# Kernel tuning notes

Hardware: AMD Instinct MI355X
Metric: run time of the kernel (lower is better)

## Reference

```python
import jax, jax.numpy as jnp
import numpy as np

WINDOW = 16      # window_size[0]
LANDM_H = 8      # closest_square_factors(64) = (8, 8)
LANDM_W = 8
MAX_VAL = 5.0
PINV_ITERS = 6


def activ(x):
    # ExpLinearAfterThreshold: exp(clamp(x, max=5)) + relu(x - 5)
    return jnp.exp(jnp.minimum(x, MAX_VAL)) + jax.nn.relu(x - MAX_VAL)


def pool_landmarks(x):
    # x: [B, H, N, d] with N = WINDOW*WINDOW.
    B, H, N, d = x.shape
    kh, kw = WINDOW // LANDM_H, WINDOW // LANDM_W
    x = x.reshape(B, H, LANDM_H, kh, LANDM_W, kw, d)
    return x.mean(axis=(3, 5)).reshape(B, H, LANDM_H * LANDM_W, d)  # [B, H, L, d]


def moore_penrose_pinv(x, iters=PINV_ITERS):
    # x: [B, H, L, L]
    abs_x = jnp.abs(x)
    col = abs_x.sum(axis=-1)
    row = abs_x.sum(axis=-2)
    z = jnp.swapaxes(x, -1, -2) / (jnp.max(col) * jnp.max(row) + 1e-15)
    I = jnp.eye(x.shape[-1], dtype=x.dtype)
    for _ in range(iters):
        xz = x @ z
        z = 0.25 * z @ (13.0 * I - xz @ (15.0 * I - xz @ (7.0 * I - xz)))
    return z


def setup_inputs() -> dict:
    key = jax.random.key(0)
    kq, kk, kv = jax.random.split(key, 3)
    shape = (256, 16, 256, 64)  # [B_, num_heads, window^2, head_dim]
    q = jax.random.normal(kq, shape, dtype=jnp.float32)
    k = jax.random.normal(kk, shape, dtype=jnp.float32)
    v = jax.random.normal(kv, shape, dtype=jnp.float32)
    return {"q": q, "k": k, "v": v}


def reference(q, k, v):
    # q, k, v: [B, H, N, d]
    q_m = pool_landmarks(q)  # [B, H, L, d]
    k_m = pool_landmarks(k)  # [B, H, L, d]

    temp = activ(jnp.einsum('bhld,bhmd->bhlm', q_m, k_m))   # [B, H, L, L]
    pinv = moore_penrose_pinv(temp, PINV_ITERS)              # [B, H, L, L]

    # kernel(q_m, k) @ [v | 1]  -> [B, H, L, d+1]
    v1 = jnp.concatenate([v, jnp.ones_like(v[..., :1])], axis=-1)
    kv = jnp.einsum('bhln,bhne->bhle', activ(jnp.einsum('bhld,bhnd->bhln', q_m, k)), v1)

    # kernel(q, k_m) @ pinv @ kv  -> [B, H, N, d+1]
    qk = activ(jnp.einsum('bhnd,bhld->bhnl', q, k_m))        # [B, H, N, L]
    prod = jnp.einsum('bhnl,bhle->bhne', qk @ pinv, kv)

    return prod[..., :-1] / (prod[..., -1:] + 1e-12)
```

## Files before the change

kernel.cpp:

```cpp
#include <hip/hip_runtime.h>
#include <math.h>


#define G_TOT 4096
#define TPB_R 256
#define TPB_M 1024
typedef _Float16 f16;
typedef __attribute__((ext_vector_type(2))) _Float16 f16x2;
typedef __attribute__((ext_vector_type(4))) _Float16 f16x4;
typedef __attribute__((ext_vector_type(8))) _Float16 f16x8;
typedef __attribute__((ext_vector_type(4))) float f32x4;
typedef __attribute__((ext_vector_type(16))) float f32x16;

#define NPLANES 16
#define SMEM_BYTES (NPLANES * 4096 * 2 + 320 * 4)

#define LSCALE 2048.0f
#define LINV   (1.0f / 2048.0f)
#define ZS     1024.0f
#define ZINV   (1.0f / 1024.0f)

struct HL { f16 h, l; };
__device__ __forceinline__ HL split2(float v) {
    HL r;
    r.h = (f16)v;
    r.l = (f16)((v - (float)r.h) * LSCALE);
    return r;
}
__device__ __forceinline__ float join2(f16 h, f16 l) {
    return (float)h + (float)l * LINV;
}
__device__ __forceinline__ int swi(int r, int c) {
    return (r << 6) + (c ^ ((r & 7) << 3));
}
__device__ __forceinline__ float activ_f(float x) {
    return __expf(fminf(x, 5.0f)) + fmaxf(x - 5.0f, 0.0f);
}
__device__ __forceinline__ float activ_r(float x) {
    return expf(fminf(x, 5.0f)) + fmaxf(x - 5.0f, 0.0f);
}
__device__ __forceinline__ void split_w(f16* Ph, f16* Pl, int r, int c, float v) {
    HL s = split2(v);
    const int o = swi(r, c);
    Ph[o] = s.h;
    Pl[o] = s.l;
}
__device__ __forceinline__ f16x2 mk2(f16 a, f16 b) { f16x2 r; r[0]=a; r[1]=b; return r; }
__device__ __forceinline__ f16x4 mk4(f16 a, f16 b, f16 c, f16 d) { f16x4 r; r[0]=a;r[1]=b;r[2]=c;r[3]=d; return r; }
__device__ __forceinline__ f32x4 z4() { f32x4 z = {0.f,0.f,0.f,0.f}; return z; }
__device__ __forceinline__ f32x16 z16() {
    f32x16 z;
#pragma unroll
    for (int i = 0; i < 16; ++i) z[i] = 0.f;
    return z;
}

struct Frag { f16x8 h[2], l[2]; };

__device__ __forceinline__ Frag ld_frag(const f16* __restrict__ Ph,
                                        const f16* __restrict__ Pl,
                                        int row, int kg) {
    Frag f;
    const int base = row << 6, x = (row & 7) << 3;
#pragma unroll
    for (int s = 0; s < 2; ++s) {
        const int o = base + ((((s << 5) + (kg << 3))) ^ x);
        f.h[s] = *(const f16x8*)(Ph + o);
        f.l[s] = *(const f16x8*)(Pl + o);
    }
    return f;
}

__device__ __forceinline__ f32x4 mm16_rr(const Frag& A, const Frag& B, f32x4 acc) {
    f32x4 ax1 = z4(), ax2 = z4();
#pragma unroll
    for (int s = 0; s < 2; ++s) {
        acc = __builtin_amdgcn_mfma_f32_16x16x32_f16(A.h[s], B.h[s], acc, 0, 0, 0);
        ax1 = __builtin_amdgcn_mfma_f32_16x16x32_f16(A.h[s], B.l[s], ax1, 0, 0, 0);
        ax2 = __builtin_amdgcn_mfma_f32_16x16x32_f16(A.l[s], B.h[s], ax2, 0, 0, 0);
    }
    acc += (ax1 + ax2) * LINV;
    return acc;
}

__device__ __forceinline__ void wfrag_rm(f16* Ph, f16* Pl, int Rb, int C, const float* v) {
#pragma unroll
    for (int m = 0; m < 4; ++m) split_w(Ph, Pl, Rb + m, C, v[m]);
}
__device__ __forceinline__ void wfrag_t(f16* Ph, f16* Pl, int Rb, int C, const float* v) {
    const int o = swi(C, Rb);
    HL s0 = split2(v[0]), s1 = split2(v[1]), s2 = split2(v[2]), s3 = split2(v[3]);
    *(f16x4*)(Ph + o) = mk4(s0.h, s1.h, s2.h, s3.h);
    *(f16x4*)(Pl + o) = mk4(s0.l, s1.l, s2.l, s3.l);
}

__device__ __forceinline__ void wr_rm(float4 vv, f16* Ph, f16* Pl, int t) {
    const int r = t >> 4, c4 = (t & 15) << 2;
    const int o = swi(r, c4);
    HL s0 = split2(vv.x), s1 = split2(vv.y), s2 = split2(vv.z), s3 = split2(vv.w);
    *(f16x4*)(Ph + o) = mk4(s0.h, s1.h, s2.h, s3.h);
    *(f16x4*)(Pl + o) = mk4(s0.l, s1.l, s2.l, s3.l);
}
__device__ __forceinline__ void ld_vt(const float* __restrict__ src, int t,
                                      float2& va, float2& vb) {
    const int n0 = (t >> 5) << 1, e0 = (t & 31) << 1;
    va = *(const float2*)(src + (size_t)n0 * 64 + e0);
    vb = *(const float2*)(src + (size_t)(n0 + 1) * 64 + e0);
}
__device__ __forceinline__ void wr_vt(float2 va, float2 vb, f16* Ph, f16* Pl, int t) {
    const int n0 = (t >> 5) << 1, e0 = (t & 31) << 1;
    HL ax = split2(va.x), ay = split2(va.y), bx = split2(vb.x), by = split2(vb.y);
    const int o0 = swi(e0, n0), o1 = swi(e0 + 1, n0);
    *(f16x2*)(Ph + o0) = mk2(ax.h, bx.h);
    *(f16x2*)(Pl + o0) = mk2(ax.l, bx.l);
    *(f16x2*)(Ph + o1) = mk2(ay.h, by.h);
    *(f16x2*)(Pl + o1) = mk2(ay.l, by.l);
}

__device__ __forceinline__ void pool_global1024(const float* __restrict__ src,
                                                f16* Ph, f16* Pl, int t) {
    const int L = t >> 4, d0 = (t & 15) << 2;
    const int nb = ((L >> 3) << 5) + ((L & 7) << 1);
    const float* p = src + (size_t)nb * 64 + d0;
    float4 a = *(const float4*)p;
    float4 b = *(const float4*)(p + 64);
    float4 c = *(const float4*)(p + 1024);
    float4 d = *(const float4*)(p + 1088);
    HL s0 = split2(0.25f * (a.x + b.x + c.x + d.x));
    HL s1 = split2(0.25f * (a.y + b.y + c.y + d.y));
    HL s2 = split2(0.25f * (a.z + b.z + c.z + d.z));
    HL s3 = split2(0.25f * (a.w + b.w + c.w + d.w));
    const int o = swi(L, d0);
    *(f16x4*)(Ph + o) = mk4(s0.h, s1.h, s2.h, s3.h);
    *(f16x4*)(Pl + o) = mk4(s0.l, s1.l, s2.l, s3.l);
}

__device__ __forceinline__ void pool_lds512(const f16* Kh, const f16* Kl,
                                            f16* Ph, f16* Pl, int t, int tt) {
    const int ll = t >> 5, d0 = (t & 31) << 1;
    const int rb = ((ll >> 3) << 5) + ((ll & 7) << 1);
    float s0 = 0.f, s1 = 0.f;
#pragma unroll
    for (int rr = 0; rr < 4; ++rr) {
        const int r = rb + (rr & 1) + ((rr >> 1) << 4);
        const int o = swi(r, d0);
        f16x2 h = *(const f16x2*)(Kh + o);
        f16x2 l = *(const f16x2*)(Kl + o);
        s0 += join2(h[0], l[0]);
        s1 += join2(h[1], l[1]);
    }
    const int L = (tt << 4) + ll;
    HL p0 = split2(0.25f * s0), p1 = split2(0.25f * s1);
    const int o = swi(L, d0);
    *(f16x2*)(Ph + o) = mk2(p0.h, p1.h);
    *(f16x2*)(Pl + o) = mk2(p0.l, p1.l);
}

__device__ __forceinline__ f32x16 mm64q(const f16* __restrict__ Ah, const f16* __restrict__ Al,
                                        const f16* __restrict__ Bh, const f16* __restrict__ Bl,
                                        int lane, int wr, int wc, f32x16 acc) {
    const int cl = lane & 31, hh = lane >> 5;
    const int ar = (wr << 5) + cl, br = (wc << 5) + cl;
    const int abase = ar << 6, axor = (ar & 7) << 3;
    const int bbase = br << 6, bxor = (br & 7) << 3;
    f32x16 ax1 = z16();
    f32x16 ax2 = z16();
#pragma unroll
    for (int ks = 0; ks < 4; ++ks) {
        const int k0 = (ks << 4) + (hh << 3);
        const int ao = abase + (k0 ^ axor);
        const int bo = bbase + (k0 ^ bxor);
        f16x8 a_h = *(const f16x8*)(Ah + ao);
        f16x8 a_l = *(const f16x8*)(Al + ao);
        f16x8 b_h = *(const f16x8*)(Bh + bo);
        f16x8 b_l = *(const f16x8*)(Bl + bo);
        acc = __builtin_amdgcn_mfma_f32_32x32x16_f16(a_h, b_h, acc, 0, 0, 0);
        ax1 = __builtin_amdgcn_mfma_f32_32x32x16_f16(a_h, b_l, ax1, 0, 0, 0);
        ax2 = __builtin_amdgcn_mfma_f32_32x32x16_f16(a_l, b_h, ax2, 0, 0, 0);
    }
    acc += (ax1 + ax2) * LINV;
    return acc;
}
__device__ __forceinline__ void pool_global_r(const float* __restrict__ src,
                                              f16* Ph, f16* Pl, int t) {
    const int ll = t >> 4, d0 = (t & 15) << 2;
    const int rb = ((ll >> 3) << 5) + ((ll & 7) << 1);
#pragma unroll
    for (int tt = 0; tt < 4; ++tt) {
        const float* p = src + (size_t)((tt << 6) + rb) * 64 + d0;
        float4 a = *(const float4*)p;
        float4 b = *(const float4*)(p + 64);
        float4 c = *(const float4*)(p + 1024);
        float4 d = *(const float4*)(p + 1088);
        const int L = (tt << 4) + ll;
        split_w(Ph, Pl, L, d0 + 0, 0.25f * (a.x + b.x + c.x + d.x));
        split_w(Ph, Pl, L, d0 + 1, 0.25f * (a.y + b.y + c.y + d.y));
        split_w(Ph, Pl, L, d0 + 2, 0.25f * (a.z + b.z + c.z + d.z));
        split_w(Ph, Pl, L, d0 + 3, 0.25f * (a.w + b.w + c.w + d.w));
    }
}

#define WAVE_SUM32(v)            \
    v += __shfl_xor(v, 1);       \
    v += __shfl_xor(v, 2);       \
    v += __shfl_xor(v, 4);       \
    v += __shfl_xor(v, 8);       \
    v += __shfl_xor(v, 16);

__global__ void k_init(float* ws) {
    if (threadIdx.x < 2) ws[threadIdx.x] = 0.0f;
}

__global__ __launch_bounds__(TPB_R) void k_reduce(const float* __restrict__ q,
                                                  const float* __restrict__ k,
                                                  float* __restrict__ ws) {
    __shared__ f16 pls[4 * 4096];
    __shared__ float rowS[64], colS[64];
    const int t = threadIdx.x, g = blockIdx.x;
    const int lane = t & 63, wv = t >> 6, wr = wv >> 1, wc = wv & 1;
    const int cl = lane & 31, hh = lane >> 5;
    if (t < 64) rowS[t] = 0.f;
    else if (t < 128) colS[t - 64] = 0.f;
    pool_global_r(q + (size_t)g * 16384, pls, pls + 4096, t);
    pool_global_r(k + (size_t)g * 16384, pls + 8192, pls + 12288, t);
    __syncthreads();
    f32x16 a = mm64q(pls, pls + 4096, pls + 8192, pls + 12288, lane, wr, wc, z16());
    float colp = 0.f;
#pragma unroll
    for (int m = 0; m < 16; ++m) {
        float x = activ_r(a[m]);
        const int R = (wr << 5) + (m & 3) + ((m >> 2) << 3) + (hh << 2);
        float vs = x;
        WAVE_SUM32(vs)
        if (cl == 0) atomicAdd(&rowS[R], vs);
        colp += x;
    }
    colp += __shfl_xor(colp, 32);
    if (hh == 0) atomicAdd(&colS[(wc << 5) + cl], colp);
    __syncthreads();
    if (t < 64) {
        float vmx = rowS[t];
        for (int off = 1; off < 64; off <<= 1) vmx = fmaxf(vmx, __shfl_xor(vmx, off));
        if (t == 0) atomicMax((int*)ws, __float_as_int(vmx));
    } else if (t < 128) {
        float vmx = colS[t - 64];
        for (int off = 1; off < 64; off <<= 1) vmx = fmaxf(vmx, __shfl_xor(vmx, off));
        if (t == 64) atomicMax(((int*)ws) + 1, __float_as_int(vmx));
    }
}

__global__ __launch_bounds__(TPB_M, 4) void k_main(const float* __restrict__ q,
                                                   const float* __restrict__ k,
                                                   const float* __restrict__ v,
                                                   const float* __restrict__ ws,
                                                   float* __restrict__ out) {
    extern __shared__ f16 smu[];
    float* kv1 = (float*)(smu + NPLANES * 4096);
    float* den = kv1 + 64;
    const int t = threadIdx.x, g = blockIdx.x;
    const int lane = t & 63, w = t >> 6;
    const int ti = w & 3, tj = w >> 2;
    const int fr = lane & 15, kg = lane >> 4;
    const int arow = (ti << 4) + fr;
    const int brow = (tj << 4) + fr;
    const int C = brow;
    const int Rb = (ti << 4) + (kg << 2);
    const float* Gq = q + (size_t)g * 16384;
    const float* Gk = k + (size_t)g * 16384;
    const float* Gv = v + (size_t)g * 16384;
    float* og = out + (size_t)g * 16384;

    f16* Xh  = smu +  0 * 4096; f16* Xl  = smu +  1 * 4096;
    f16* SAh = smu +  2 * 4096; f16* SAl = smu +  3 * 4096;
    f16* SBh = smu +  4 * 4096; f16* SBl = smu +  5 * 4096;
    f16* KMh = smu +  6 * 4096; f16* KMl = smu +  7 * 4096;
    f16* SCh = smu +  8 * 4096; f16* SCl = smu +  9 * 4096;
    f16* KVh = smu + 10 * 4096; f16* KVl = smu + 11 * 4096;
    f16* Z0rh= smu + 12 * 4096; f16* Z0rl= smu + 13 * 4096;
    f16* Z0th= smu + 14 * 4096; f16* Z0tl= smu + 15 * 4096;

    if (t < 320) kv1[t] = 0.f;
    pool_global1024(Gq, Z0rh, Z0rl, t);
    {
        float4 kreg = *(const float4*)(Gk + (size_t)t * 4);
        float2 va, vb; ld_vt(Gv, t, va, vb);
        wr_rm(kreg, SAh, SAl, t);
        wr_vt(va, vb, SBh, SBl, t);
    }
    __syncthreads();

    Frag fQM = ld_frag(Z0rh, Z0rl, arow, kg);

    f32x4 kva = z4();
    for (int tt = 0; tt < 4; ++tt) {
        f16* vch = (tt & 1) ? Xh : SBh;  f16* vcl = (tt & 1) ? Xl : SBl;
        f16* vnh = (tt & 1) ? SBh : Xh;  f16* vnl = (tt & 1) ? SBl : Xl;
        float4 kregN; float2 vaN, vbN;
        if (tt < 3) {
            kregN = *(const float4*)(Gk + (size_t)(tt + 1) * 4096 + (size_t)t * 4);
            ld_vt(Gv + (size_t)(tt + 1) * 4096, t, vaN, vbN);
        }
        if (t < 512) pool_lds512(SAh, SAl, KMh, KMl, t, tt);
        {
            Frag bK = ld_frag(SAh, SAl, brow, kg);
            f32x4 s = mm16_rr(fQM, bK, z4());
            float sv[4];
#pragma unroll
            for (int m = 0; m < 4; ++m) {
                sv[m] = activ_f(s[m]);
                float vs = sv[m];
                vs += __shfl_xor(vs, 1); vs += __shfl_xor(vs, 2);
                vs += __shfl_xor(vs, 4); vs += __shfl_xor(vs, 8);
                if (fr == 0) atomicAdd(&kv1[Rb + m], vs);
            }
            wfrag_rm(SCh, SCl, Rb, C, sv);
        }
        if (tt < 3) wr_vt(vaN, vbN, vnh, vnl, t);
        __syncthreads();
        {
            Frag aS = ld_frag(SCh, SCl, arow, kg);
            Frag bV = ld_frag(vch, vcl, brow, kg);
            kva = mm16_rr(aS, bV, kva);
        }
        if (tt < 3) wr_rm(kregN, SAh, SAl, t);
        __syncthreads();
    }

    {
        float kvv[4] = {kva[0], kva[1], kva[2], kva[3]};
        wfrag_t(KVh, KVl, Rb, C, kvv);
        Frag fKMb = ld_frag(KMh, KMl, brow, kg);
        f32x4 x0 = mm16_rr(fQM, fKMb, z4());
        const float scale = ZS / (ws[0] * ws[1] + 1e-15f);
        float xv[4], zv[4];
#pragma unroll
        for (int m = 0; m < 4; ++m) { xv[m] = activ_f(x0[m]); zv[m] = xv[m] * scale; }
        wfrag_rm(Xh, Xl, Rb, C, xv);
        wfrag_t (Z0rh, Z0rl, Rb, C, zv);
        wfrag_rm(Z0th, Z0tl, Rb, C, zv);
    }
    __syncthreads();

    Frag fX = ld_frag(Xh, Xl, arow, kg);
    f16 *zrh = Z0rh, *zrl = Z0rl, *zth = Z0th, *ztl = Z0tl;
    f16 *nrh = SAh,  *nrl = SAl,  *nth = SCh,  *ntl = SCl;
#pragma unroll
    for (int it = 0; it < 6; ++it) {
        Frag bz = ld_frag(zth, ztl, brow, kg);
        f32x4 a1 = mm16_rr(fX, bz, z4());
        float t1k[4];
#pragma unroll
        for (int m = 0; m < 4; ++m) t1k[m] = a1[m] * ZINV;
        wfrag_rm(nrh, nrl, Rb, C, t1k);
        wfrag_t (nth, ntl, Rb, C, t1k);
        __syncthreads();
        Frag aT1 = ld_frag(nrh, nrl, arow, kg);
        Frag bT1 = ld_frag(nth, ntl, brow, kg);
        f32x4 a2 = mm16_rr(aT1, bT1, z4());
        float t2k[4];
#pragma unroll
        for (int m = 0; m < 4; ++m) t2k[m] = a2[m];
        wfrag_rm(Xh, Xl, Rb, C, t2k);
        __syncthreads();
        Frag aT2 = ld_frag(Xh, Xl, arow, kg);
        f32x4 a3 = mm16_rr(aT2, bT1, z4());
        float ov[4];
#pragma unroll
        for (int m = 0; m < 4; ++m) {
            const int R = Rb + m;
            ov[m] = ((R == C) ? 13.f : 0.f) - 15.f * t1k[m] + 7.f * t2k[m] - a3[m];
        }
        wfrag_t(SBh, SBl, Rb, C, ov);
        __syncthreads();
        Frag aZ = ld_frag(zrh, zrl, arow, kg);
        Frag bO = ld_frag(SBh, SBl, brow, kg);
        f32x4 a4 = mm16_rr(aZ, bO, z4());
        float zk[4];
#pragma unroll
        for (int m = 0; m < 4; ++m) zk[m] = 0.25f * a4[m];
        wfrag_rm(nrh, nrl, Rb, C, zk);
        wfrag_t (nth, ntl, Rb, C, zk);
        __syncthreads();
        f16* tp;
        tp = zrh; zrh = nrh; nrh = tp;  tp = zrl; zrl = nrl; nrl = tp;
        tp = zth; zth = nth; nth = tp;  tp = ztl; ztl = ntl; ntl = tp;
    }

    Frag fKM = ld_frag(KMh, KMl, brow, kg);
    Frag fZt = ld_frag(Z0th, Z0tl, brow, kg);
    Frag fKV = ld_frag(KVh, KVl, brow, kg);
    const float kvC = kv1[C];
    {
        float4 qreg = *(const float4*)(Gq + (size_t)t * 4);
        wr_rm(qreg, SAh, SAl, t);
    }
    __syncthreads();
    for (int tt = 0; tt < 4; ++tt) {
        float4 qregN;
        if (tt < 3) qregN = *(const float4*)(Gq + (size_t)(tt + 1) * 4096 + (size_t)t * 4);
        {
            Frag aQ = ld_frag(SAh, SAl, arow, kg);
            f32x4 q0 = mm16_rr(aQ, fKM, z4());
            float qv[4];
#pragma unroll
            for (int m = 0; m < 4; ++m) qv[m] = activ_f(q0[m]);
            wfrag_rm(SCh, SCl, Rb, C, qv);
        }
        __syncthreads();
        float* dn = den + (tt << 6);
        {
            Frag aK = ld_frag(SCh, SCl, arow, kg);
            f32x4 w0 = mm16_rr(aK, fZt, z4());
            float wv[4];
#pragma unroll
            for (int m = 0; m < 4; ++m) {
                wv[m] = w0[m] * ZINV;
                float d_ = wv[m] * kvC;
                d_ += __shfl_xor(d_, 1); d_ += __shfl_xor(d_, 2);
                d_ += __shfl_xor(d_, 4); d_ += __shfl_xor(d_, 8);
                if (fr == 0) atomicAdd(&dn[Rb + m], d_);
            }
            wfrag_rm(SBh, SBl, Rb, C, wv);
        }
        __syncthreads();
        {
            Frag aW = ld_frag(SBh, SBl, arow, kg);
            f32x4 p0 = mm16_rr(aW, fKV, z4());
#pragma unroll
            for (int m = 0; m < 4; ++m) {
                const int R = Rb + m;
                const float inv = 1.0f / (dn[R] + 1e-12f);
                og[(size_t)((tt << 6) + R) * 64 + C] = p0[m] * inv;
            }
        }
        if (tt < 3) wr_rm(qregN, SAh, SAl, t);
        __syncthreads();
    }
}

extern "C" void kernel_launch(void* const* d_in, const int* in_sizes, int n_in,
                              void* d_out, int out_size, void* d_ws, size_t ws_size,
                              hipStream_t stream) {
    const float* q = (const float*)d_in[0];
    const float* k = (const float*)d_in[1];
    const float* v = (const float*)d_in[2];
    float* out = (float*)d_out;
    float* ws  = (float*)d_ws;
    (void)in_sizes; (void)n_in; (void)out_size; (void)ws_size;

    hipFuncSetAttribute((const void*)k_main,
                        hipFuncAttributeMaxDynamicSharedMemorySize, SMEM_BYTES);

    k_init<<<1, 64, 0, stream>>>(ws);
    k_reduce<<<G_TOT, TPB_R, 0, stream>>>(q, k, ws);
    k_main<<<G_TOT, TPB_M, SMEM_BYTES, stream>>>(q, k, v, ws, out);
}
```

Measured before the change: 768.5 us.

## Process two 64-row chunks per stage to halve barrier count

The KV accumulation and output phases now handle two 64-row token chunks at once instead of looping over four chunks one at a time. Pairs of fragments are computed per barrier using spare LDS planes (SC, KV, Zt, X) as extra staging buffers. This cuts the number of __syncthreads and exposes more independent MFMA work per stage. In exchange it raises register pressure and loads more global data up front.

```diff
diff --git a/kernel.cpp b/kernel.cpp
--- a/kernel.cpp
+++ b/kernel.cpp
@@ -276,55 +276,96 @@
     f16* KMh = smu +  6 * 4096; f16* KMl = smu +  7 * 4096;
     f16* SCh = smu +  8 * 4096; f16* SCl = smu +  9 * 4096;
     f16* KVh = smu + 10 * 4096; f16* KVl = smu + 11 * 4096;
-    f16* Z0rh= smu + 12 * 4096; f16* Z0rl= smu + 13 * 4096;
-    f16* Z0th= smu + 14 * 4096; f16* Z0tl= smu + 15 * 4096;
+    f16* Zrh = smu + 12 * 4096; f16* Zrl = smu + 13 * 4096;
+    f16* Zth = smu + 14 * 4096; f16* Ztl = smu + 15 * 4096;
 
     if (t < 320) kv1[t] = 0.f;
-    pool_global1024(Gq, Z0rh, Z0rl, t);
-    {
-        float4 kreg = *(const float4*)(Gk + (size_t)t * 4);
-        float2 va, vb; ld_vt(Gv, t, va, vb);
-        wr_rm(kreg, SAh, SAl, t);
-        wr_vt(va, vb, SBh, SBl, t);
-    }
-    __syncthreads();
-
-    Frag fQM = ld_frag(Z0rh, Z0rl, arow, kg);
+    pool_global1024(Gq, Zrh, Zrl, t);
+    {
+        float4 k0 = *(const float4*)(Gk + (size_t)t * 4);
+        float4 k1 = *(const float4*)(Gk + 4096 + (size_t)t * 4);
+        float2 va0, vb0, va1, vb1;
+        ld_vt(Gv, t, va0, vb0);
+        ld_vt(Gv + 4096, t, va1, vb1);
+        wr_rm(k0, SAh, SAl, t);
+        wr_rm(k1, SCh, SCl, t);
+        wr_vt(va0, vb0, SBh, SBl, t);
+        wr_vt(va1, vb1, Xh, Xl, t);
+    }
+    __syncthreads();
+
+    Frag fQM = ld_frag(Zrh, Zrl, arow, kg);
 
     f32x4 kva = z4();
-    for (int tt = 0; tt < 4; ++tt) {
-        f16* vch = (tt & 1) ? Xh : SBh;  f16* vcl = (tt & 1) ? Xl : SBl;
-        f16* vnh = (tt & 1) ? SBh : Xh;  f16* vnl = (tt & 1) ? SBl : Xl;
-        float4 kregN; float2 vaN, vbN;
-        if (tt < 3) {
-            kregN = *(const float4*)(Gk + (size_t)(tt + 1) * 4096 + (size_t)t * 4);
-            ld_vt(Gv + (size_t)(tt + 1) * 4096, t, vaN, vbN);
-        }
-        if (t < 512) pool_lds512(SAh, SAl, KMh, KMl, t, tt);
-        {
-            Frag bK = ld_frag(SAh, SAl, brow, kg);
-            f32x4 s = mm16_rr(fQM, bK, z4());
-            float sv[4];
-#pragma unroll
-            for (int m = 0; m < 4; ++m) {
-                sv[m] = activ_f(s[m]);
-                float vs = sv[m];
-                vs += __shfl_xor(vs, 1); vs += __shfl_xor(vs, 2);
-                vs += __shfl_xor(vs, 4); vs += __shfl_xor(vs, 8);
-                if (fr == 0) atomicAdd(&kv1[Rb + m], vs);
-            }
-            wfrag_rm(SCh, SCl, Rb, C, sv);
-        }
-        if (tt < 3) wr_vt(vaN, vbN, vnh, vnl, t);
-        __syncthreads();
-        {
-            Frag aS = ld_frag(SCh, SCl, arow, kg);
-            Frag bV = ld_frag(vch, vcl, brow, kg);
-            kva = mm16_rr(aS, bV, kva);
-        }
-        if (tt < 3) wr_rm(kregN, SAh, SAl, t);
-        __syncthreads();
-    }
+    float4 kr2 = *(const float4*)(Gk + 2 * 4096 + (size_t)t * 4);
+    float4 kr3 = *(const float4*)(Gk + 3 * 4096 + (size_t)t * 4);
+    if (t < 512) pool_lds512(SAh, SAl, KMh, KMl, t, 0);
+    else         pool_lds512(SCh, SCl, KMh, KMl, t - 512, 1);
+    {
+        Frag b0 = ld_frag(SAh, SAl, brow, kg);
+        Frag b1 = ld_frag(SCh, SCl, brow, kg);
+        f32x4 s0 = mm16_rr(fQM, b0, z4());
+        f32x4 s1 = mm16_rr(fQM, b1, z4());
+        float sv0[4], sv1[4];
+#pragma unroll
+        for (int m = 0; m < 4; ++m) {
+            sv0[m] = activ_f(s0[m]);
+            sv1[m] = activ_f(s1[m]);
+            float vs = sv0[m] + sv1[m];
+            vs += __shfl_xor(vs, 1); vs += __shfl_xor(vs, 2);
+            vs += __shfl_xor(vs, 4); vs += __shfl_xor(vs, 8);
+            if (fr == 0) atomicAdd(&kv1[Rb + m], vs);
+        }
+        wfrag_rm(Zth, Ztl, Rb, C, sv0);
+        wfrag_rm(KVh, KVl, Rb, C, sv1);
+    }
+    __syncthreads();
+    float2 va2, vb2, va3, vb3;
+    ld_vt(Gv + 2 * 4096, t, va2, vb2);
+    ld_vt(Gv + 3 * 4096, t, va3, vb3);
+    {
+        Frag a0 = ld_frag(Zth, Ztl, arow, kg);
+        Frag b0 = ld_frag(SBh, SBl, brow, kg);
+        kva = mm16_rr(a0, b0, kva);
+        Frag a1 = ld_frag(KVh, KVl, arow, kg);
+        Frag b1 = ld_frag(Xh, Xl, brow, kg);
+        kva = mm16_rr(a1, b1, kva);
+    }
+    wr_rm(kr2, SAh, SAl, t);
+    wr_rm(kr3, SCh, SCl, t);
+    __syncthreads();
+    if (t < 512) pool_lds512(SAh, SAl, KMh, KMl, t, 2);
+    else         pool_lds512(SCh, SCl, KMh, KMl, t - 512, 3);
+    {
+        Frag b0 = ld_frag(SAh, SAl, brow, kg);
+        Frag b1 = ld_frag(SCh, SCl, brow, kg);
+        f32x4 s0 = mm16_rr(fQM, b0, z4());
+        f32x4 s1 = mm16_rr(fQM, b1, z4());
+        float sv0[4], sv1[4];
+#pragma unroll
+        for (int m = 0; m < 4; ++m) {
+            sv0[m] = activ_f(s0[m]);
+            sv1[m] = activ_f(s1[m]);
+            float vs = sv0[m] + sv1[m];
+            vs += __shfl_xor(vs, 1); vs += __shfl_xor(vs, 2);
+            vs += __shfl_xor(vs, 4); vs += __shfl_xor(vs, 8);
+            if (fr == 0) atomicAdd(&kv1[Rb + m], vs);
+        }
+        wfrag_rm(Zth, Ztl, Rb, C, sv0);
+        wfrag_rm(KVh, KVl, Rb, C, sv1);
+    }
+    wr_vt(va2, vb2, SBh, SBl, t);
+    wr_vt(va3, vb3, Xh, Xl, t);
+    __syncthreads();
+    {
+        Frag a0 = ld_frag(Zth, Ztl, arow, kg);
+        Frag b0 = ld_frag(SBh, SBl, brow, kg);
+        kva = mm16_rr(a0, b0, kva);
+        Frag a1 = ld_frag(KVh, KVl, arow, kg);
+        Frag b1 = ld_frag(Xh, Xl, brow, kg);
+        kva = mm16_rr(a1, b1, kva);
+    }
+    __syncthreads();
 
     {
         float kvv[4] = {kva[0], kva[1], kva[2], kva[3]};
@@ -336,14 +377,14 @@
 #pragma unroll
         for (int m = 0; m < 4; ++m) { xv[m] = activ_f(x0[m]); zv[m] = xv[m] * scale; }
         wfrag_rm(Xh, Xl, Rb, C, xv);
-        wfrag_t (Z0rh, Z0rl, Rb, C, zv);
-        wfrag_rm(Z0th, Z0tl, Rb, C, zv);
+        wfrag_t (Zrh, Zrl, Rb, C, zv);
+        wfrag_rm(Zth, Ztl, Rb, C, zv);
     }
     __syncthreads();
 
     Frag fX = ld_frag(Xh, Xl, arow, kg);
-    f16 *zrh = Z0rh, *zrl = Z0rl, *zth = Z0th, *ztl = Z0tl;
-    f16 *nrh = SAh,  *nrl = SAl,  *nth = SCh,  *ntl = SCl;
+    f16 *zrh = Zrh, *zrl = Zrl, *zth = Zth, *ztl = Ztl;
+    f16 *nrh = SAh, *nrl = SAl, *nth = SCh, *ntl = SCl;
 #pragma unroll
     for (int it = 0; it < 6; ++it) {
         Frag bz = ld_frag(zth, ztl, brow, kg);
@@ -386,55 +427,115 @@
         tp = zth; zth = nth; nth = tp;  tp = ztl; ztl = ntl; ntl = tp;
     }
 
+    {
+        float4 q0 = *(const float4*)(Gq + (size_t)t * 4);
+        float4 q1 = *(const float4*)(Gq + 4096 + (size_t)t * 4);
+        wr_rm(q0, SAh, SAl, t);
+        wr_rm(q1, SCh, SCl, t);
+    }
     Frag fKM = ld_frag(KMh, KMl, brow, kg);
-    Frag fZt = ld_frag(Z0th, Z0tl, brow, kg);
+    Frag fZt = ld_frag(Zth, Ztl, brow, kg);
     Frag fKV = ld_frag(KVh, KVl, brow, kg);
     const float kvC = kv1[C];
-    {
-        float4 qreg = *(const float4*)(Gq + (size_t)t * 4);
-        wr_rm(qreg, SAh, SAl, t);
-    }
-    __syncthreads();
-    for (int tt = 0; tt < 4; ++tt) {
-        float4 qregN;
-        if (tt < 3) qregN = *(const float4*)(Gq + (size_t)(tt + 1) * 4096 + (size_t)t * 4);
-        {
-            Frag aQ = ld_frag(SAh, SAl, arow, kg);
-            f32x4 q0 = mm16_rr(aQ, fKM, z4());
-            float qv[4];
-#pragma unroll
-            for (int m = 0; m < 4; ++m) qv[m] = activ_f(q0[m]);
-            wfrag_rm(SCh, SCl, Rb, C, qv);
-        }
-        __syncthreads();
-        float* dn = den + (tt << 6);
-        {
-            Frag aK = ld_frag(SCh, SCl, arow, kg);
-            f32x4 w0 = mm16_rr(aK, fZt, z4());
-            float wv[4];
-#pragma unroll
-            for (int m = 0; m < 4; ++m) {
-                wv[m] = w0[m] * ZINV;
-                float d_ = wv[m] * kvC;
-                d_ += __shfl_xor(d_, 1); d_ += __shfl_xor(d_, 2);
-                d_ += __shfl_xor(d_, 4); d_ += __shfl_xor(d_, 8);
-                if (fr == 0) atomicAdd(&dn[Rb + m], d_);
-            }
-            wfrag_rm(SBh, SBl, Rb, C, wv);
-        }
-        __syncthreads();
-        {
-            Frag aW = ld_frag(SBh, SBl, arow, kg);
-            f32x4 p0 = mm16_rr(aW, fKV, z4());
-#pragma unroll
-            for (int m = 0; m < 4; ++m) {
-                const int R = Rb + m;
-                const float inv = 1.0f / (dn[R] + 1e-12f);
-                og[(size_t)((tt << 6) + R) * 64 + C] = p0[m] * inv;
-            }
-        }
-        if (tt < 3) wr_rm(qregN, SAh, SAl, t);
-        __syncthreads();
+    float4 qr2 = *(const float4*)(Gq + 2 * 4096 + (size_t)t * 4);
+    float4 qr3 = *(const float4*)(Gq + 3 * 4096 + (size_t)t * 4);
+    __syncthreads();
+    {
+        Frag a0 = ld_frag(SAh, SAl, arow, kg);
+        Frag a1 = ld_frag(SCh, SCl, arow, kg);
+        f32x4 r0 = mm16_rr(a0, fKM, z4());
+        f32x4 r1 = mm16_rr(a1, fKM, z4());
+        float qv0[4], qv1[4];
+#pragma unroll
+        for (int m = 0; m < 4; ++m) { qv0[m] = activ_f(r0[m]); qv1[m] = activ_f(r1[m]); }
+        wfrag_rm(SBh, SBl, Rb, C, qv0);
+        wfrag_rm(Xh, Xl, Rb, C, qv1);
+    }
+    __syncthreads();
+    {
+        Frag a0 = ld_frag(SBh, SBl, arow, kg);
+        Frag a1 = ld_frag(Xh, Xl, arow, kg);
+        f32x4 w0 = mm16_rr(a0, fZt, z4());
+        f32x4 w1 = mm16_rr(a1, fZt, z4());
+        float wv0[4], wv1[4];
+#pragma unroll
+        for (int m = 0; m < 4; ++m) {
+            wv0[m] = w0[m] * ZINV;
+            wv1[m] = w1[m] * ZINV;
+            float d0_ = wv0[m] * kvC;
+            d0_ += __shfl_xor(d0_, 1); d0_ += __shfl_xor(d0_, 2);
+            d0_ += __shfl_xor(d0_, 4); d0_ += __shfl_xor(d0_, 8);
+            if (fr == 0) atomicAdd(&den[Rb + m], d0_);
+            float d1_ = wv1[m] * kvC;
+            d1_ += __shfl_xor(d1_, 1); d1_ += __shfl_xor(d1_, 2);
+            d1_ += __shfl_xor(d1_, 4); d1_ += __shfl_xor(d1_, 8);
+            if (fr == 0) atomicAdd(&den[64 + Rb + m], d1_);
+        }
+        wfrag_rm(SAh, SAl, Rb, C, wv0);
+        wfrag_rm(SCh, SCl, Rb, C, wv1);
+    }
+    __syncthreads();
+    {
+        Frag a0 = ld_frag(SAh, SAl, arow, kg);
+        Frag a1 = ld_frag(SCh, SCl, arow, kg);
+        f32x4 p0 = mm16_rr(a0, fKV, z4());
+        f32x4 p1 = mm16_rr(a1, fKV, z4());
+#pragma unroll
+        for (int m = 0; m < 4; ++m) {
+            const int R = Rb + m;
+            og[(size_t)R * 64 + C]         = p0[m] / (den[R] + 1e-12f);
+            og[(size_t)(64 + R) * 64 + C]  = p1[m] / (den[64 + R] + 1e-12f);
+        }
+    }
+    wr_rm(qr2, SBh, SBl, t);
+    wr_rm(qr3, Xh, Xl, t);
+    __syncthreads();
+    {
+        Frag a0 = ld_frag(SBh, SBl, arow, kg);
+        Frag a1 = ld_frag(Xh, Xl, arow, kg);
+        f32x4 r0 = mm16_rr(a0, fKM, z4());
+        f32x4 r1 = mm16_rr(a1, fKM, z4());
+        float qv0[4], qv1[4];
+#pragma unroll
+        for (int m = 0; m < 4; ++m) { qv0[m] = activ_f(r0[m]); qv1[m] = activ_f(r1[m]); }
+        wfrag_rm(SAh, SAl, Rb, C, qv0);
+        wfrag_rm(SCh, SCl, Rb, C, qv1);
+    }
+    __syncthreads();
+    {
+        Frag a0 = ld_frag(SAh, SAl, arow, kg);
+        Frag a1 = ld_frag(SCh, SCl, arow, kg);
+        f32x4 w0 = mm16_rr(a0, fZt, z4());
+        f32x4 w1 = mm16_rr(a1, fZt, z4());
+        float wv0[4], wv1[4];
+#pragma unroll
+        for (int m = 0; m < 4; ++m) {
+            wv0[m] = w0[m] * ZINV;
+            wv1[m] = w1[m] * ZINV;
+            float d0_ = wv0[m] * kvC;
+            d0_ += __shfl_xor(d0_, 1); d0_ += __shfl_xor(d0_, 2);
+            d0_ += __shfl_xor(d0_, 4); d0_ += __shfl_xor(d0_, 8);
+            if (fr == 0) atomicAdd(&den[128 + Rb + m], d0_);
+            float d1_ = wv1[m] * kvC;
+            d1_ += __shfl_xor(d1_, 1); d1_ += __shfl_xor(d1_, 2);
+            d1_ += __shfl_xor(d1_, 4); d1_ += __shfl_xor(d1_, 8);
+            if (fr == 0) atomicAdd(&den[192 + Rb + m], d1_);
+        }
+        wfrag_rm(SBh, SBl, Rb, C, wv0);
+        wfrag_rm(Xh, Xl, Rb, C, wv1);
+    }
+    __syncthreads();
+    {
+        Frag a0 = ld_frag(SBh, SBl, arow, kg);
+        Frag a1 = ld_frag(Xh, Xl, arow, kg);
+        f32x4 p0 = mm16_rr(a0, fKV, z4());
+        f32x4 p1 = mm16_rr(a1, fKV, z4());
+#pragma unroll
+        for (int m = 0; m < 4; ++m) {
+            const int R = Rb + m;
+            og[(size_t)(128 + R) * 64 + C] = p0[m] / (den[128 + R] + 1e-12f);
+            og[(size_t)(192 + R) * 64 + C] = p1[m] / (den[192 + R] + 1e-12f);
+        }
     }
 }
 
```

Result: slower. 802.8 us (+4.5%).

## Shrink LDS footprint to ten planes for two blocks per CU

Applied to the files above, without the earlier changes.

Cuts the shared-memory layout from sixteen planes to ten by reusing buffers across phases. The pooled K landmarks and the kv accumulator are parked in the block's own output region and reloaded later. The final stage builds Q fragments straight from global memory, and the LDS atomics for row sums and denominators become per-wave partials reduced through shared memory. Launch bounds are raised so two 1024-thread blocks can share a CU. The cost is extra global traffic, one more barrier per tile, and a tighter register budget that may cause spills.

```diff
diff --git a/kernel.cpp b/kernel.cpp
--- a/kernel.cpp
+++ b/kernel.cpp
@@ -12,8 +12,8 @@
 typedef __attribute__((ext_vector_type(4))) float f32x4;
 typedef __attribute__((ext_vector_type(16))) float f32x16;
 
-#define NPLANES 16
-#define SMEM_BYTES (NPLANES * 4096 * 2 + 320 * 4)
+#define NPLANES 10
+#define SMEM_BYTES (NPLANES * 4096 * 2)
 
 #define LSCALE 2048.0f
 #define LINV   (1.0f / 2048.0f)
@@ -67,6 +67,25 @@
         const int o = base + ((((s << 5) + (kg << 3))) ^ x);
         f.h[s] = *(const f16x8*)(Ph + o);
         f.l[s] = *(const f16x8*)(Pl + o);
+    }
+    return f;
+}
+
+__device__ __forceinline__ Frag mk_gfrag(const float* __restrict__ row, int kg) {
+    Frag f;
+#pragma unroll
+    for (int s = 0; s < 2; ++s) {
+        const float* p = row + (s << 5) + (kg << 3);
+        float4 a = *(const float4*)p;
+        float4 b = *(const float4*)(p + 4);
+        float vv0 = a.x, vv1 = a.y, vv2 = a.z, vv3 = a.w;
+        float vv4 = b.x, vv5 = b.y, vv6 = b.z, vv7 = b.w;
+        HL s0 = split2(vv0), s1 = split2(vv1), s2 = split2(vv2), s3 = split2(vv3);
+        HL s4 = split2(vv4), s5 = split2(vv5), s6 = split2(vv6), s7 = split2(vv7);
+        f16x8 h, l;
+        h[0]=s0.h; h[1]=s1.h; h[2]=s2.h; h[3]=s3.h; h[4]=s4.h; h[5]=s5.h; h[6]=s6.h; h[7]=s7.h;
+        l[0]=s0.l; l[1]=s1.l; l[2]=s2.l; l[3]=s3.l; l[4]=s4.l; l[5]=s5.l; l[6]=s6.l; l[7]=s7.l;
+        f.h[s] = h; f.l[s] = l;
     }
     return f;
 }
@@ -116,7 +135,6 @@
     *(f16x2*)(Ph + o1) = mk2(ay.h, by.h);
     *(f16x2*)(Pl + o1) = mk2(ay.l, by.l);
 }
-
 __device__ __forceinline__ void pool_global1024(const float* __restrict__ src,
                                                 f16* Ph, f16* Pl, int t) {
     const int L = t >> 4, d0 = (t & 15) << 2;
@@ -134,7 +152,6 @@
     *(f16x4*)(Ph + o) = mk4(s0.h, s1.h, s2.h, s3.h);
     *(f16x4*)(Pl + o) = mk4(s0.l, s1.l, s2.l, s3.l);
 }
-
 __device__ __forceinline__ void pool_lds512(const f16* Kh, const f16* Kl,
                                             f16* Ph, f16* Pl, int t, int tt) {
     const int ll = t >> 5, d0 = (t & 31) << 1;
@@ -249,14 +266,19 @@
     }
 }
 
-__global__ __launch_bounds__(TPB_M, 4) void k_main(const float* __restrict__ q,
+__global__ __launch_bounds__(TPB_M, 8) void k_main(const float* __restrict__ q,
                                                    const float* __restrict__ k,
                                                    const float* __restrict__ v,
                                                    const float* __restrict__ ws,
                                                    float* __restrict__ out) {
     extern __shared__ f16 smu[];
-    float* kv1 = (float*)(smu + NPLANES * 4096);
-    float* den = kv1 + 64;
+    f16* P1h = smu;            f16* P1l = smu + 4096;
+    f16* P2h = smu + 8192;     f16* P2l = smu + 12288;
+    f16* P3h = smu + 16384;    f16* P3l = smu + 20480;
+    f16* P4h = smu + 24576;    f16* P4l = smu + 28672;
+    f16* P5h = smu + 32768;    f16* P5l = smu + 36864;
+    float* P5f = (float*)P5h;
+
     const int t = threadIdx.x, g = blockIdx.x;
     const int lane = t & 63, w = t >> 6;
     const int ti = w & 3, tj = w >> 2;
@@ -270,39 +292,30 @@
     const float* Gv = v + (size_t)g * 16384;
     float* og = out + (size_t)g * 16384;
 
-    f16* Xh  = smu +  0 * 4096; f16* Xl  = smu +  1 * 4096;
-    f16* SAh = smu +  2 * 4096; f16* SAl = smu +  3 * 4096;
-    f16* SBh = smu +  4 * 4096; f16* SBl = smu +  5 * 4096;
-    f16* KMh = smu +  6 * 4096; f16* KMl = smu +  7 * 4096;
-    f16* SCh = smu +  8 * 4096; f16* SCl = smu +  9 * 4096;
-    f16* KVh = smu + 10 * 4096; f16* KVl = smu + 11 * 4096;
-    f16* Z0rh= smu + 12 * 4096; f16* Z0rl= smu + 13 * 4096;
-    f16* Z0th= smu + 14 * 4096; f16* Z0tl= smu + 15 * 4096;
-
-    if (t < 320) kv1[t] = 0.f;
-    pool_global1024(Gq, Z0rh, Z0rl, t);
+    pool_global1024(Gq, P5h, P5l, t);
     {
-        float4 kreg = *(const float4*)(Gk + (size_t)t * 4);
-        float2 va, vb; ld_vt(Gv, t, va, vb);
-        wr_rm(kreg, SAh, SAl, t);
-        wr_vt(va, vb, SBh, SBl, t);
-    }
-    __syncthreads();
-
-    Frag fQM = ld_frag(Z0rh, Z0rl, arow, kg);
+        float4 k0 = *(const float4*)(Gk + (size_t)t * 4);
+        float2 va0, vb0; ld_vt(Gv, t, va0, vb0);
+        wr_rm(k0, P1h, P1l, t);
+        wr_vt(va0, vb0, P2h, P2l, t);
+    }
+    __syncthreads();
+
+    Frag fQM = ld_frag(P5h, P5l, arow, kg);
 
     f32x4 kva = z4();
+    float kv1p[4] = {0.f, 0.f, 0.f, 0.f};
     for (int tt = 0; tt < 4; ++tt) {
-        f16* vch = (tt & 1) ? Xh : SBh;  f16* vcl = (tt & 1) ? Xl : SBl;
-        f16* vnh = (tt & 1) ? SBh : Xh;  f16* vnl = (tt & 1) ? SBl : Xl;
-        float4 kregN; float2 vaN, vbN;
+        f16* ch = (tt & 1) ? P5h : P2h; f16* cl_ = (tt & 1) ? P5l : P2l;
+        f16* nh = (tt & 1) ? P2h : P5h; f16* nl = (tt & 1) ? P2l : P5l;
+        float4 krN; float2 vaN, vbN;
         if (tt < 3) {
-            kregN = *(const float4*)(Gk + (size_t)(tt + 1) * 4096 + (size_t)t * 4);
+            krN = *(const float4*)(Gk + (size_t)(tt + 1) * 4096 + (size_t)t * 4);
             ld_vt(Gv + (size_t)(tt + 1) * 4096, t, vaN, vbN);
         }
-        if (t < 512) pool_lds512(SAh, SAl, KMh, KMl, t, tt);
+        if (t < 512) pool_lds512(P1h, P1l, P4h, P4l, t, tt);
         {
-            Frag bK = ld_frag(SAh, SAl, brow, kg);
+            Frag bK = ld_frag(P1h, P1l, brow, kg);
             f32x4 s = mm16_rr(fQM, bK, z4());
             float sv[4];
 #pragma unroll
@@ -311,58 +324,73 @@
                 float vs = sv[m];
                 vs += __shfl_xor(vs, 1); vs += __shfl_xor(vs, 2);
                 vs += __shfl_xor(vs, 4); vs += __shfl_xor(vs, 8);
-                if (fr == 0) atomicAdd(&kv1[Rb + m], vs);
+                kv1p[m] += vs;
             }
-            wfrag_rm(SCh, SCl, Rb, C, sv);
-        }
-        if (tt < 3) wr_vt(vaN, vbN, vnh, vnl, t);
+            wfrag_rm(P3h, P3l, Rb, C, sv);
+        }
         __syncthreads();
         {
-            Frag aS = ld_frag(SCh, SCl, arow, kg);
-            Frag bV = ld_frag(vch, vcl, brow, kg);
+            Frag aS = ld_frag(P3h, P3l, arow, kg);
+            Frag bV = ld_frag(ch, cl_, brow, kg);
             kva = mm16_rr(aS, bV, kva);
         }
-        if (tt < 3) wr_rm(kregN, SAh, SAl, t);
+        if (tt < 3) {
+            wr_rm(krN, P1h, P1l, t);
+            wr_vt(vaN, vbN, nh, nl, t);
+        }
         __syncthreads();
     }
 
     {
-        float kvv[4] = {kva[0], kva[1], kva[2], kva[3]};
-        wfrag_t(KVh, KVl, Rb, C, kvv);
-        Frag fKMb = ld_frag(KMh, KMl, brow, kg);
+        const unsigned* sKM = (const unsigned*)P4h;
+        unsigned* dKM = (unsigned*)og;
+#pragma unroll
+        for (int i = 0; i < 4; ++i) dKM[t + (i << 10)] = sKM[t + (i << 10)];
+#pragma unroll
+        for (int m = 0; m < 4; ++m) og[4096 + (size_t)(Rb + m) * 64 + C] = kva[m];
+        Frag fKMb = ld_frag(P4h, P4l, brow, kg);
         f32x4 x0 = mm16_rr(fQM, fKMb, z4());
         const float scale = ZS / (ws[0] * ws[1] + 1e-15f);
         float xv[4], zv[4];
 #pragma unroll
         for (int m = 0; m < 4; ++m) { xv[m] = activ_f(x0[m]); zv[m] = xv[m] * scale; }
-        wfrag_rm(Xh, Xl, Rb, C, xv);
-        wfrag_t (Z0rh, Z0rl, Rb, C, zv);
-        wfrag_rm(Z0th, Z0tl, Rb, C, zv);
-    }
-    __syncthreads();
-
-    Frag fX = ld_frag(Xh, Xl, arow, kg);
-    f16 *zrh = Z0rh, *zrl = Z0rl, *zth = Z0th, *ztl = Z0tl;
-    f16 *nrh = SAh,  *nrl = SAl,  *nth = SCh,  *ntl = SCl;
+        wfrag_rm(P1h, P1l, Rb, C, xv);
+        wfrag_t (P2h, P2l, Rb, C, zv);
+        wfrag_rm(P3h, P3l, Rb, C, zv);
+    }
+    __syncthreads();
+
+    Frag fX = ld_frag(P1h, P1l, arow, kg);
+    if (fr == 0) {
+#pragma unroll
+        for (int m = 0; m < 4; ++m) P5f[(tj << 6) + Rb + m] = kv1p[m];
+    }
+    __syncthreads();
+
+    f16 *r0h = P2h, *r0l = P2l;
+    f16 *r1h = P4h, *r1l = P4l;
+    f16 *r2h = P5h, *r2l = P5l;
+    float kvC = 0.f;
 #pragma unroll
     for (int it = 0; it < 6; ++it) {
-        Frag bz = ld_frag(zth, ztl, brow, kg);
+        Frag bz = ld_frag(P3h, P3l, brow, kg);
         f32x4 a1 = mm16_rr(fX, bz, z4());
+        if (it == 0) kvC = P5f[C] + P5f[64 + C] + P5f[128 + C] + P5f[192 + C];
         float t1k[4];
 #pragma unroll
         for (int m = 0; m < 4; ++m) t1k[m] = a1[m] * ZINV;
-        wfrag_rm(nrh, nrl, Rb, C, t1k);
-        wfrag_t (nth, ntl, Rb, C, t1k);
-        __syncthreads();
-        Frag aT1 = ld_frag(nrh, nrl, arow, kg);
-        Frag bT1 = ld_frag(nth, ntl, brow, kg);
+        wfrag_rm(P1h, P1l, Rb, C, t1k);
+        wfrag_t (r1h, r1l, Rb, C, t1k);
+        __syncthreads();
+        Frag aT1 = ld_frag(P1h, P1l, arow, kg);
+        Frag bT1 = ld_frag(r1h, r1l, brow, kg);
         f32x4 a2 = mm16_rr(aT1, bT1, z4());
         float t2k[4];
 #pragma unroll
         for (int m = 0; m < 4; ++m) t2k[m] = a2[m];
-        wfrag_rm(Xh, Xl, Rb, C, t2k);
-        __syncthreads();
-        Frag aT2 = ld_frag(Xh, Xl, arow, kg);
+        wfrag_rm(r2h, r2l, Rb, C, t2k);
+        __syncthreads();
+        Frag aT2 = ld_frag(r2h, r2l, arow, kg);
         f32x4 a3 = mm16_rr(aT2, bT1, z4());
         float ov[4];
 #pragma unroll
@@ -370,47 +398,54 @@
             const int R = Rb + m;
             ov[m] = ((R == C) ? 13.f : 0.f) - 15.f * t1k[m] + 7.f * t2k[m] - a3[m];
         }
-        wfrag_t(SBh, SBl, Rb, C, ov);
-        __syncthreads();
-        Frag aZ = ld_frag(zrh, zrl, arow, kg);
-        Frag bO = ld_frag(SBh, SBl, brow, kg);
+        wfrag_t(P1h, P1l, Rb, C, ov);
+        __syncthreads();
+        Frag aZ = ld_frag(r0h, r0l, arow, kg);
+        Frag bO = ld_frag(P1h, P1l, brow, kg);
         f32x4 a4 = mm16_rr(aZ, bO, z4());
         float zk[4];
 #pragma unroll
         for (int m = 0; m < 4; ++m) zk[m] = 0.25f * a4[m];
-        wfrag_rm(nrh, nrl, Rb, C, zk);
-        wfrag_t (nth, ntl, Rb, C, zk);
-        __syncthreads();
-        f16* tp;
-        tp = zrh; zrh = nrh; nrh = tp;  tp = zrl; zrl = nrl; nrl = tp;
-        tp = zth; zth = nth; nth = tp;  tp = ztl; ztl = ntl; ntl = tp;
-    }
-
-    Frag fKM = ld_frag(KMh, KMl, brow, kg);
-    Frag fZt = ld_frag(Z0th, Z0tl, brow, kg);
-    Frag fKV = ld_frag(KVh, KVl, brow, kg);
-    const float kvC = kv1[C];
+        wfrag_rm(r1h, r1l, Rb, C, zk);
+        wfrag_t (P3h, P3l, Rb, C, zk);
+        __syncthreads();
+        f16 *th, *tl;
+        th = r0h; tl = r0l;
+        r0h = r1h; r0l = r1l;
+        r1h = r2h; r1l = r2l;
+        r2h = th;  r2l = tl;
+    }
+
     {
-        float4 qreg = *(const float4*)(Gq + (size_t)t * 4);
-        wr_rm(qreg, SAh, SAl, t);
-    }
-    __syncthreads();
+        const unsigned* sKM = (const unsigned*)og;
+        unsigned* dKM = (unsigned*)P1h;
+#pragma unroll
+        for (int i = 0; i < 4; ++i) dKM[t + (i << 10)] = sKM[t + (i << 10)];
+        float4 kvv = *(const float4*)(og + 4096 + (size_t)t * 4);
+        const int l = t >> 4, e0 = (t & 15) << 2;
+        split_w(P4h, P4l, e0 + 0, l, kvv.x);
+        split_w(P4h, P4l, e0 + 1, l, kvv.y);
+        split_w(P4h, P4l, e0 + 2, l, kvv.z);
+        split_w(P4h, P4l, e0 + 3, l, kvv.w);
+    }
+    __syncthreads();
+
     for (int tt = 0; tt < 4; ++tt) {
-        float4 qregN;
-        if (tt < 3) qregN = *(const float4*)(Gq + (size_t)(tt + 1) * 4096 + (size_t)t * 4);
         {
-            Frag aQ = ld_frag(SAh, SAl, arow, kg);
-            f32x4 q0 = mm16_rr(aQ, fKM, z4());
+            Frag aQ = mk_gfrag(Gq + (size_t)((tt << 6) + arow) * 64, kg);
+            Frag bKM = ld_frag(P1h, P1l, brow, kg);
+            f32x4 q0 = mm16_rr(aQ, bKM, z4());
             float qv[4];
 #pragma unroll
             for (int m = 0; m < 4; ++m) qv[m] = activ_f(q0[m]);
-            wfrag_rm(SCh, SCl, Rb, C, qv);
-        }
-        __syncthreads();
-        float* dn = den + (tt << 6);
+            wfrag_rm(P5h, P5l, Rb, C, qv);
+        }
+        __syncthreads();
+        float dp[4];
         {
-            Frag aK = ld_frag(SCh, SCl, arow, kg);
-            f32x4 w0 = mm16_rr(aK, fZt, z4());
+            Frag aK = ld_frag(P5h, P5l, arow, kg);
+            Frag bZt = ld_frag(P3h, P3l, brow, kg);
+            f32x4 w0 = mm16_rr(aK, bZt, z4());
             float wv[4];
 #pragma unroll
             for (int m = 0; m < 4; ++m) {
@@ -418,22 +453,27 @@
                 float d_ = wv[m] * kvC;
                 d_ += __shfl_xor(d_, 1); d_ += __shfl_xor(d_, 2);
                 d_ += __shfl_xor(d_, 4); d_ += __shfl_xor(d_, 8);
-                if (fr == 0) atomicAdd(&dn[Rb + m], d_);
+                dp[m] = d_;
             }
-            wfrag_rm(SBh, SBl, Rb, C, wv);
+            wfrag_rm(P2h, P2l, Rb, C, wv);
+        }
+        __syncthreads();
+        if (fr == 0) {
+#pragma unroll
+            for (int m = 0; m < 4; ++m) P5f[(tj << 6) + Rb + m] = dp[m];
         }
         __syncthreads();
         {
-            Frag aW = ld_frag(SBh, SBl, arow, kg);
-            f32x4 p0 = mm16_rr(aW, fKV, z4());
+            Frag aW = ld_frag(P2h, P2l, arow, kg);
+            Frag bKV = ld_frag(P4h, P4l, brow, kg);
+            f32x4 p0 = mm16_rr(aW, bKV, z4());
 #pragma unroll
             for (int m = 0; m < 4; ++m) {
                 const int R = Rb + m;
-                const float inv = 1.0f / (dn[R] + 1e-12f);
-                og[(size_t)((tt << 6) + R) * 64 + C] = p0[m] * inv;
+                const float den = P5f[R] + P5f[64 + R] + P5f[128 + R] + P5f[192 + R];
+                og[(size_t)((tt << 6) + R) * 64 + C] = p0[m] / (den + 1e-12f);
             }
         }
-        if (tt < 3) wr_rm(qregN, SAh, SAl, t);
         __syncthreads();
     }
 }
```

Result: slower. 1.680 ms (+118.6%).

## Compute row sums and denominators via MFMA instead of shuffle-atomic reductions

Applied to the files above, without the earlier changes.

Drops the wave-shuffle plus LDS atomicAdd reductions for the kv ones-column and the final denominators. Both are now computed with extra MFMAs: against an all-ones fragment, and against a fragment built from kv1. Q tiles in the final phase are loaded straight from global memory into MFMA fragments, skipping the LDS staging. The two cross-term accumulators in mm16_rr are merged into one. The cost is more MFMA work and duplicated denominator computation across waves. Reading Q per lane from global may also give less coalesced access.

```diff
diff --git a/kernel.cpp b/kernel.cpp
--- a/kernel.cpp
+++ b/kernel.cpp
@@ -13,7 +13,7 @@
 typedef __attribute__((ext_vector_type(16))) float f32x16;
 
 #define NPLANES 16
-#define SMEM_BYTES (NPLANES * 4096 * 2 + 320 * 4)
+#define SMEM_BYTES (NPLANES * 4096 * 2 + 64 * 4)
 
 #define LSCALE 2048.0f
 #define LINV   (1.0f / 2048.0f)
@@ -72,14 +72,14 @@
 }
 
 __device__ __forceinline__ f32x4 mm16_rr(const Frag& A, const Frag& B, f32x4 acc) {
-    f32x4 ax1 = z4(), ax2 = z4();
+    f32x4 ax = z4();
 #pragma unroll
     for (int s = 0; s < 2; ++s) {
         acc = __builtin_amdgcn_mfma_f32_16x16x32_f16(A.h[s], B.h[s], acc, 0, 0, 0);
-        ax1 = __builtin_amdgcn_mfma_f32_16x16x32_f16(A.h[s], B.l[s], ax1, 0, 0, 0);
-        ax2 = __builtin_amdgcn_mfma_f32_16x16x32_f16(A.l[s], B.h[s], ax2, 0, 0, 0);
-    }
-    acc += (ax1 + ax2) * LINV;
+        ax  = __builtin_amdgcn_mfma_f32_16x16x32_f16(A.h[s], B.l[s], ax, 0, 0, 0);
+        ax  = __builtin_amdgcn_mfma_f32_16x16x32_f16(A.l[s], B.h[s], ax, 0, 0, 0);
+    }
+    acc += ax * LINV;
     return acc;
 }
 
@@ -116,7 +116,6 @@
     *(f16x2*)(Ph + o1) = mk2(ay.h, by.h);
     *(f16x2*)(Pl + o1) = mk2(ay.l, by.l);
 }
-
 __device__ __forceinline__ void pool_global1024(const float* __restrict__ src,
                                                 f16* Ph, f16* Pl, int t) {
     const int L = t >> 4, d0 = (t & 15) << 2;
@@ -134,7 +133,6 @@
     *(f16x4*)(Ph + o) = mk4(s0.h, s1.h, s2.h, s3.h);
     *(f16x4*)(Pl + o) = mk4(s0.l, s1.l, s2.l, s3.l);
 }
-
 __device__ __forceinline__ void pool_lds512(const f16* Kh, const f16* Kl,
                                             f16* Ph, f16* Pl, int t, int tt) {
     const int ll = t >> 5, d0 = (t & 31) << 1;
@@ -256,7 +254,6 @@
                                                    float* __restrict__ out) {
     extern __shared__ f16 smu[];
     float* kv1 = (float*)(smu + NPLANES * 4096);
-    float* den = kv1 + 64;
     const int t = threadIdx.x, g = blockIdx.x;
     const int lane = t & 63, w = t >> 6;
     const int ti = w & 3, tj = w >> 2;
@@ -279,7 +276,15 @@
     f16* Z0rh= smu + 12 * 4096; f16* Z0rl= smu + 13 * 4096;
     f16* Z0th= smu + 14 * 4096; f16* Z0tl= smu + 15 * 4096;
 
-    if (t < 320) kv1[t] = 0.f;
+    Frag fOnes;
+    {
+        f16x8 one8, zer8;
+#pragma unroll
+        for (int i = 0; i < 8; ++i) { one8[i] = (f16)1.0f; zer8[i] = (f16)0.0f; }
+        fOnes.h[0] = one8; fOnes.h[1] = one8;
+        fOnes.l[0] = zer8; fOnes.l[1] = zer8;
+    }
+
     pool_global1024(Gq, Z0rh, Z0rl, t);
     {
         float4 kreg = *(const float4*)(Gk + (size_t)t * 4);
@@ -292,6 +297,7 @@
     Frag fQM = ld_frag(Z0rh, Z0rl, arow, kg);
 
     f32x4 kva = z4();
+    f32x4 kva1 = z4();
     for (int tt = 0; tt < 4; ++tt) {
         f16* vch = (tt & 1) ? Xh : SBh;  f16* vcl = (tt & 1) ? Xl : SBl;
         f16* vnh = (tt & 1) ? SBh : Xh;  f16* vnl = (tt & 1) ? SBl : Xl;
@@ -306,13 +312,7 @@
             f32x4 s = mm16_rr(fQM, bK, z4());
             float sv[4];
 #pragma unroll
-            for (int m = 0; m < 4; ++m) {
-                sv[m] = activ_f(s[m]);
-                float vs = sv[m];
-                vs += __shfl_xor(vs, 1); vs += __shfl_xor(vs, 2);
-                vs += __shfl_xor(vs, 4); vs += __shfl_xor(vs, 8);
-                if (fr == 0) atomicAdd(&kv1[Rb + m], vs);
-            }
+            for (int m = 0; m < 4; ++m) sv[m] = activ_f(s[m]);
             wfrag_rm(SCh, SCl, Rb, C, sv);
         }
         if (tt < 3) wr_vt(vaN, vbN, vnh, vnl, t);
@@ -320,7 +320,8 @@
         {
             Frag aS = ld_frag(SCh, SCl, arow, kg);
             Frag bV = ld_frag(vch, vcl, brow, kg);
-            kva = mm16_rr(aS, bV, kva);
+            kva  = mm16_rr(aS, bV, kva);
+            kva1 = mm16_rr(aS, fOnes, kva1);
         }
         if (tt < 3) wr_rm(kregN, SAh, SAl, t);
         __syncthreads();
@@ -338,6 +339,10 @@
         wfrag_rm(Xh, Xl, Rb, C, xv);
         wfrag_t (Z0rh, Z0rl, Rb, C, zv);
         wfrag_rm(Z0th, Z0tl, Rb, C, zv);
+        if (tj == 0 && fr == 0) {
+#pragma unroll
+            for (int m = 0; m < 4; ++m) kv1[Rb + m] = kva1[m];
+        }
     }
     __syncthreads();
 
@@ -389,17 +394,44 @@
     Frag fKM = ld_frag(KMh, KMl, brow, kg);
     Frag fZt = ld_frag(Z0th, Z0tl, brow, kg);
     Frag fKV = ld_frag(KVh, KVl, brow, kg);
-    const float kvC = kv1[C];
-    {
-        float4 qreg = *(const float4*)(Gq + (size_t)t * 4);
-        wr_rm(qreg, SAh, SAl, t);
-    }
-    __syncthreads();
+    Frag fKv1;
+#pragma unroll
+    for (int s = 0; s < 2; ++s) {
+        const float* kp = kv1 + (s << 5) + (kg << 3);
+        float4 A = *(const float4*)kp;
+        float4 B = *(const float4*)(kp + 4);
+        HL s0 = split2(A.x), s1 = split2(A.y), s2 = split2(A.z), s3 = split2(A.w);
+        HL s4 = split2(B.x), s5 = split2(B.y), s6 = split2(B.z), s7 = split2(B.w);
+        f16x8 h, l;
+        h[0]=s0.h; h[1]=s1.h; h[2]=s2.h; h[3]=s3.h; h[4]=s4.h; h[5]=s5.h; h[6]=s6.h; h[7]=s7.h;
+        l[0]=s0.l; l[1]=s1.l; l[2]=s2.l; l[3]=s3.l; l[4]=s4.l; l[5]=s5.l; l[6]=s6.l; l[7]=s7.l;
+        fKv1.h[s] = h; fKv1.l[s] = l;
+    }
+    float4 qp0, qp1, qp2, qp3;
+#define LOAD_Q(tt_)                                                              \
+    {                                                                            \
+        const float* rp = Gq + (size_t)(((tt_) << 6) + arow) * 64 + (kg << 3);   \
+        qp0 = *(const float4*)(rp);      qp1 = *(const float4*)(rp + 4);         \
+        qp2 = *(const float4*)(rp + 32); qp3 = *(const float4*)(rp + 36);        \
+    }
+    LOAD_Q(0)
     for (int tt = 0; tt < 4; ++tt) {
-        float4 qregN;
-        if (tt < 3) qregN = *(const float4*)(Gq + (size_t)(tt + 1) * 4096 + (size_t)t * 4);
         {
-            Frag aQ = ld_frag(SAh, SAl, arow, kg);
+            Frag aQ;
+            {
+                HL s0 = split2(qp0.x), s1 = split2(qp0.y), s2 = split2(qp0.z), s3 = split2(qp0.w);
+                HL s4 = split2(qp1.x), s5 = split2(qp1.y), s6 = split2(qp1.z), s7 = split2(qp1.w);
+                f16x8 h, l;
+                h[0]=s0.h; h[1]=s1.h; h[2]=s2.h; h[3]=s3.h; h[4]=s4.h; h[5]=s5.h; h[6]=s6.h; h[7]=s7.h;
+                l[0]=s0.l; l[1]=s1.l; l[2]=s2.l; l[3]=s3.l; l[4]=s4.l; l[5]=s5.l; l[6]=s6.l; l[7]=s7.l;
+                aQ.h[0] = h; aQ.l[0] = l;
+                HL t0 = split2(qp2.x), t1 = split2(qp2.y), t2 = split2(qp2.z), t3 = split2(qp2.w);
+                HL t4 = split2(qp3.x), t5 = split2(qp3.y), t6 = split2(qp3.z), t7 = split2(qp3.w);
+                f16x8 h2, l2;
+                h2[0]=t0.h; h2[1]=t1.h; h2[2]=t2.h; h2[3]=t3.h; h2[4]=t4.h; h2[5]=t5.h; h2[6]=t6.h; h2[7]=t7.h;
+                l2[0]=t0.l; l2[1]=t1.l; l2[2]=t2.l; l2[3]=t3.l; l2[4]=t4.l; l2[5]=t5.l; l2[6]=t6.l; l2[7]=t7.l;
+                aQ.h[1] = h2; aQ.l[1] = l2;
+            }
             f32x4 q0 = mm16_rr(aQ, fKM, z4());
             float qv[4];
 #pragma unroll
@@ -407,35 +439,30 @@
             wfrag_rm(SCh, SCl, Rb, C, qv);
         }
         __syncthreads();
-        float* dn = den + (tt << 6);
         {
             Frag aK = ld_frag(SCh, SCl, arow, kg);
             f32x4 w0 = mm16_rr(aK, fZt, z4());
             float wv[4];
 #pragma unroll
-            for (int m = 0; m < 4; ++m) {
-                wv[m] = w0[m] * ZINV;
-                float d_ = wv[m] * kvC;
-                d_ += __shfl_xor(d_, 1); d_ += __shfl_xor(d_, 2);
-                d_ += __shfl_xor(d_, 4); d_ += __shfl_xor(d_, 8);
-                if (fr == 0) atomicAdd(&dn[Rb + m], d_);
-            }
+            for (int m = 0; m < 4; ++m) wv[m] = w0[m] * ZINV;
             wfrag_rm(SBh, SBl, Rb, C, wv);
         }
+        if (tt < 3) LOAD_Q(tt + 1)
         __syncthreads();
         {
             Frag aW = ld_frag(SBh, SBl, arow, kg);
             f32x4 p0 = mm16_rr(aW, fKV, z4());
+            f32x4 d4 = mm16_rr(aW, fKv1, z4());
 #pragma unroll
             for (int m = 0; m < 4; ++m) {
                 const int R = Rb + m;
-                const float inv = 1.0f / (dn[R] + 1e-12f);
+                const float inv = 1.0f / (d4[m] + 1e-12f);
                 og[(size_t)((tt << 6) + R) * 64 + C] = p0[m] * inv;
             }
         }
-        if (tt < 3) wr_rm(qregN, SAh, SAl, t);
-        __syncthreads();
-    }
+        __syncthreads();
+    }
+#undef LOAD_Q
 }
 
 extern "C" void kernel_launch(void* const* d_in, const int* in_sizes, int n_in,
```

After: 794.3 us. +3.4%, slower.
